# Optimization experiments

Measured on AMD Instinct MI355X. Metric: run time of the kernel, lower is better.

Reference implementation:

```python
import jax, jax.numpy as jnp
import numpy as np
from jax import lax

EPS = 1e-5
DIM = 96      # channels = dim
KS = 96       # kernel_size == H == W
GROUPS = 8
BATCH = 4
FFN_F = 2.66

# relative index table: emb[c, i, j] = rel[c, i - j + KS - 1]
_REL_IDX = (np.arange(KS)[:, None] - np.arange(KS)[None, :] + KS - 1).reshape(-1)


def _bn(x, g, b, ax):
    """BatchNorm (training-mode batch statistics) over all axes except `ax`."""
    axes = tuple(i for i in range(x.ndim) if i != ax)
    m = x.mean(axes, keepdims=True)
    v = x.var(axes, keepdims=True)
    sh = [1] * x.ndim
    sh[ax] = -1
    return (x - m) / jnp.sqrt(v + EPS) * g.reshape(sh) + b.reshape(sh)


def _ln(x, w, b):
    """WithBias LayerNorm over channel dim of NCHW (per-pixel over C)."""
    m = x.mean(1, keepdims=True)
    v = x.var(1, keepdims=True)
    return (x - m) / jnp.sqrt(v + EPS) * w[None, :, None, None] + b[None, :, None, None]


def _axial(x, wqkv, gq, bq, rel, gs, bs, go, bo, width):
    # x: (N, C, H, W)
    xp = x.transpose(0, 2, 1, 3) if width else x.transpose(0, 3, 1, 2)
    N, Wd, C, L = xp.shape
    gp = C // GROUPS  # group_planes
    xb = xp.reshape(N * Wd, C, L)
    qkv = _bn(jnp.einsum('oc,bcl->bol', wqkv, xb), gq, bq, 1)
    qkv = qkv.reshape(N * Wd, GROUPS, 2 * gp, L)
    q, k, v = qkv[:, :, :gp // 2], qkv[:, :, gp // 2:gp], qkv[:, :, gp:]
    emb = rel[:, _REL_IDX].reshape(2 * gp, L, L)
    qe, ke, ve = emb[:gp // 2], emb[gp // 2:gp], emb[gp:]
    qk = jnp.einsum('bgci,bgcj->bgij', q, k)
    qr = jnp.einsum('bgci,cij->bgij', q, qe)
    kr = jnp.einsum('bgci,cij->bgij', k, ke).transpose(0, 1, 3, 2)
    sim = _bn(jnp.concatenate([qk, qr, kr], 1), gs, bs, 1)
    sim = sim.reshape(N * Wd, 3, GROUPS, L, L).sum(1)
    sim = jax.nn.softmax(sim, axis=3)
    sv = jnp.einsum('bgij,bgcj->bgci', sim, v)
    sve = jnp.einsum('bgij,cij->bgci', sim, ve)
    out = _bn(jnp.concatenate([sv, sve], -1).reshape(N * Wd, 2 * C, L), go, bo, 1)
    out = out.reshape(N, Wd, C, 2, L).sum(3)
    return out.transpose(0, 2, 1, 3) if width else out.transpose(0, 2, 3, 1)


def _ffn(x, win, wdw, wout):
    h = jnp.einsum('oc,bchw->bohw', win, x)
    h = lax.conv_general_dilated(h, wdw, (1, 1), 'SAME',
                                 dimension_numbers=('NCHW', 'OIHW', 'NCHW'),
                                 feature_group_count=h.shape[1])
    x1, x2 = jnp.split(h, 2, axis=1)
    return jnp.einsum('oc,bchw->bohw', wout, jax.nn.gelu(x1, approximate=False) * x2)


def setup_inputs() -> dict:
    key = jax.random.key(0)
    ks = jax.random.split(key, 8)
    dim, gp = DIM, DIM // GROUPS
    hid = int(dim * FFN_F)
    f = jax.random.normal
    d = {'x': f(ks[0], (BATCH, dim, KS, KS), jnp.float32)}
    d['ln1_w'] = jnp.ones(dim); d['ln1_b'] = jnp.zeros(dim)
    for p, i in (('h_', 1), ('w_', 2)):
        k1, k2 = jax.random.split(ks[i])
        d[p + 'wqkv'] = f(k1, (2 * dim, dim), jnp.float32) * float(np.sqrt(1.0 / dim))
        d[p + 'gqkv'] = jnp.ones(2 * dim); d[p + 'bqkv'] = jnp.zeros(2 * dim)
        d[p + 'rel'] = f(k2, (2 * gp, 2 * KS - 1), jnp.float32) * float(np.sqrt(1.0 / gp))
        d[p + 'gsim'] = jnp.ones(3 * GROUPS); d[p + 'bsim'] = jnp.zeros(3 * GROUPS)
        d[p + 'gout'] = jnp.ones(2 * dim); d[p + 'bout'] = jnp.zeros(2 * dim)
    d['ln2_w'] = jnp.ones(dim); d['ln2_b'] = jnp.zeros(dim)
    d['ffn_win'] = f(ks[3], (2 * hid, dim), jnp.float32) * float(np.sqrt(1.0 / dim))
    d['ffn_wdw'] = f(ks[4], (2 * hid, 1, 3, 3), jnp.float32) * 0.1
    d['ffn_wout'] = f(ks[5], (dim, hid), jnp.float32) * float(np.sqrt(1.0 / hid))
    return d


def reference(x, ln1_w, ln1_b,
              h_wqkv, h_gqkv, h_bqkv, h_rel, h_gsim, h_bsim, h_gout, h_bout,
              w_wqkv, w_gqkv, w_bqkv, w_rel, w_gsim, w_bsim, w_gout, w_bout,
              ln2_w, ln2_b, ffn_win, ffn_wdw, ffn_wout):
    y = _ln(x, ln1_w, ln1_b)
    y = _axial(y, h_wqkv, h_gqkv, h_bqkv, h_rel, h_gsim, h_bsim, h_gout, h_bout, False)
    y = _axial(y, w_wqkv, w_gqkv, w_bqkv, w_rel, w_gsim, w_bsim, w_gout, w_bout, True)
    x = x + y
    x = x + _ffn(_ln(x, ln2_w, ln2_b), ffn_win, ffn_wdw, ffn_wout)
    return x
```

## Files before the change

### kernel.cpp

```cpp
#include <hip/hip_runtime.h>
#include <hip/hip_bf16.h>
#include <math.h>

using bf16 = __hip_bfloat16;

#define NB 4
#define C_ 96
#define NPIX 36864
#define IMG 9216
#define CH_ST 9216
#define N_ST 884736
#define HID 255
#define EPSF 1e-5f
#define TOT 3538944

__global__ __launch_bounds__(256) void ln_kernel(const float* __restrict__ X,
                                                 float* __restrict__ Y,
                                                 const float* __restrict__ w,
                                                 const float* __restrict__ b) {
  int pix = blockIdx.x * 256 + threadIdx.x;
  if (pix >= NPIX) return;
  int n = pix / IMG, p = pix % IMG;
  const float* xp = X + (long)n * N_ST + p;
  float s = 0.f, sq = 0.f;
  for (int c = 0; c < C_; c++) { float v = xp[c * CH_ST]; s += v; sq += v * v; }
  float m = s * (1.f / C_);
  float var = fmaxf(sq * (1.f / C_) - m * m, 0.f);
  float r = rsqrtf(var + EPSF);
  float* yp = Y + (long)n * N_ST + p;
  for (int c = 0; c < C_; c++)
    yp[c * CH_ST] = (xp[c * CH_ST] - m) * r * w[c] + b[c];
}

__global__ void trans_kernel(const float* __restrict__ Y0, float* __restrict__ Y0C) {
  __shared__ float T[32][33];
  int nc = blockIdx.z; int n = nc / C_, c = nc % C_;
  int h0 = blockIdx.x * 32, w0 = blockIdx.y * 32;
  int tx = threadIdx.x, ty = threadIdx.y;
  const float* src = Y0 + (long)n * N_ST + (long)c * CH_ST;
  for (int r = 0; r < 4; r++)
    T[ty + 8 * r][tx] = src[(h0 + ty + 8 * r) * 96 + w0 + tx];
  __syncthreads();
  float* dst = Y0C + (long)c * NPIX + (long)n * IMG;
  for (int r = 0; r < 4; r++)
    dst[(w0 + ty + 8 * r) * 96 + h0 + tx] = T[tx][ty + 8 * r];
}

template<int TM, int TN, int EPI>
__global__ __launch_bounds__(256) void gemm_kernel(
    const float* __restrict__ A, const float* __restrict__ B,
    float* __restrict__ Cout, int M, int K, int NperZ,
    long bCstride, long bZstride, int batch,
    const float* __restrict__ X1, float* __restrict__ OutF) {
  constexpr int NT = TN / 16;
  constexpr int RT = TM / 16;
  __shared__ float As[32][TM];
  __shared__ float Bs[32][TN + 4];
  const int tx = threadIdx.x, ty = threadIdx.y;
  const int tid = ty * 16 + tx;
  const int m0 = blockIdx.y * TM;
  const int q0 = blockIdx.x * TN;
  const int z  = blockIdx.z;
  const float* Bz = B + (long)z * bZstride;
  float acc[RT][NT];
  #pragma unroll
  for (int a = 0; a < RT; a++)
    #pragma unroll
    for (int b = 0; b < NT; b++) acc[a][b] = 0.f;

  for (int kk = 0; kk < K; kk += 32) {
    #pragma unroll
    for (int it = 0; it < (32 * TM) / 256; it++) {
      int i = tid + it * 256;
      int c = i / TM, r = i % TM;
      int mm = m0 + r, kc = kk + c;
      As[c][r] = (mm < M && kc < K) ? A[(long)mm * K + kc] : 0.f;
    }
    #pragma unroll
    for (int it = 0; it < (32 * TN) / 256; it++) {
      int i = tid + it * 256;
      int c = i / TN, q = i % TN;
      int kc = kk + c;
      Bs[c][q] = (kc < K) ? Bz[(long)kc * bCstride + q0 + q] : 0.f;
    }
    __syncthreads();
    for (int kc = 0; kc < 32; kc++) {
      float av[RT];
      if constexpr (RT % 4 == 0) {
        #pragma unroll
        for (int u = 0; u < RT / 4; u++) {
          float4 a4 = *(const float4*)&As[kc][ty * RT + 4 * u];
          av[4 * u] = a4.x; av[4 * u + 1] = a4.y; av[4 * u + 2] = a4.z; av[4 * u + 3] = a4.w;
        }
      } else {
        #pragma unroll
        for (int u = 0; u < RT / 2; u++) {
          float2 a2 = *(const float2*)&As[kc][ty * RT + 2 * u];
          av[2 * u] = a2.x; av[2 * u + 1] = a2.y;
        }
      }
      float bv[NT];
      #pragma unroll
      for (int v4 = 0; v4 < NT / 4; v4++) {
        float4 b4 = *(const float4*)&Bs[kc][v4 * 64 + tx * 4];
        bv[v4 * 4] = b4.x; bv[v4 * 4 + 1] = b4.y; bv[v4 * 4 + 2] = b4.z; bv[v4 * 4 + 3] = b4.w;
      }
      #pragma unroll
      for (int a = 0; a < RT; a++)
        #pragma unroll
        for (int b = 0; b < NT; b++)
          acc[a][b] = fmaf(av[a], bv[b], acc[a][b]);
    }
    __syncthreads();
  }
  const long oStride = (long)NperZ * gridDim.z;
  if (EPI == 0) {
    #pragma unroll
    for (int a = 0; a < RT; a++) {
      int mm = m0 + ty * RT + a;
      if (mm < M) {
        float* dst = Cout + (long)mm * oStride + (long)z * NperZ + q0;
        #pragma unroll
        for (int v4 = 0; v4 < NT / 4; v4++)
          *(float4*)(dst + v4 * 64 + tx * 4) =
              make_float4(acc[a][v4 * 4], acc[a][v4 * 4 + 1],
                          acc[a][v4 * 4 + 2], acc[a][v4 * 4 + 3]);
      }
    }
  } else {
    #pragma unroll
    for (int a = 0; a < RT; a++) {
      int mm = m0 + ty * RT + a;
      if (mm < M) {
        #pragma unroll
        for (int v4 = 0; v4 < NT / 4; v4++) {
          int Q = q0 + v4 * 64 + tx * 4;
          int n = batch + z + Q / IMG, p = Q % IMG;
          long base = (long)n * N_ST + (long)mm * CH_ST + p;
          #pragma unroll
          for (int b = 0; b < 4; b++)
            OutF[base + b] = acc[a][v4 * 4 + b] + X1[base + b];
        }
      }
    }
  }
}

__global__ __launch_bounds__(1024) void rowstat_kernel(const float* __restrict__ D,
                                                       const float* __restrict__ g,
                                                       const float* __restrict__ b,
                                                       float2* __restrict__ aff) {
  int o = blockIdx.x;
  const float4* p = (const float4*)(D + (long)o * NPIX);
  float s = 0.f, sq = 0.f;
  for (int i = threadIdx.x; i < NPIX / 4; i += 1024) {
    float4 v = p[i];
    s  += v.x + v.y + v.z + v.w;
    sq += v.x * v.x + v.y * v.y + v.z * v.z + v.w * v.w;
  }
  for (int off = 32; off; off >>= 1) { s += __shfl_down(s, off); sq += __shfl_down(sq, off); }
  __shared__ float ss[16], ssq[16];
  int wv = threadIdx.x >> 6, lane = threadIdx.x & 63;
  if (lane == 0) { ss[wv] = s; ssq[wv] = sq; }
  __syncthreads();
  if (threadIdx.x == 0) {
    float S = 0.f, SQ = 0.f;
    #pragma unroll
    for (int i = 0; i < 16; i++) { S += ss[i]; SQ += ssq[i]; }
    float m = S / (float)NPIX;
    float var = fmaxf(SQ / (float)NPIX - m * m, 0.f);
    float sc = g[o] * rsqrtf(var + EPSF);
    aff[o] = make_float2(sc, b[o] - m * sc);
  }
}

__global__ void relstat_kernel(const float* __restrict__ relp, float* __restrict__ tbl) {
  int i = threadIdx.x;
  if (i >= 96) return;
  int side = blockIdx.x / 27, row = blockIdx.x % 27;
  const float* base = relp + side * 6 * 191;
  float* T = tbl + side * 27 * 96;
  if (row < 6) {
    float s = 0.f;
    for (int d = 0; d < 96; d++) s += base[row * 191 + i + d];
    T[row * 96 + i] = s;
  } else {
    int p = row - 6, c = 0;
    while (p >= 6 - c) { p -= 6 - c; c++; }
    int c2 = c + p;
    float s = 0.f;
    for (int d = 0; d < 96; d++) s += base[c * 191 + i + d] * base[c2 * 191 + i + d];
    T[576 + (row - 6) * 96 + i] = s;
  }
}

__global__ __launch_bounds__(256) void simstat2_kernel(const float* __restrict__ QKV,
                                                       const float2* __restrict__ aff,
                                                       const float* __restrict__ tbl,
                                                       float* __restrict__ stats) {
  int g = blockIdx.x & 7, chunk = blockIdx.x >> 3;
  int bbg = threadIdx.x >> 5, lane = threadIdx.x & 31;
  int bb = chunk * 8 + bbg;
  const float* Aq = tbl;
  const float* Wq = tbl + 6 * 96;
  const float* Ak = tbl + 27 * 96;
  const float* Wk = tbl + 27 * 96 + 6 * 96;
  float Sq[6] = {}, Sk[6] = {}, Gq[21] = {}, Gk[21] = {};
  float lq = 0.f, lsq = 0.f, lk = 0.f, lsk = 0.f;
  #pragma unroll
  for (int ii = 0; ii < 3; ii++) {
    int i = lane + 32 * ii;
    float qv[6], kv[6];
    #pragma unroll
    for (int c = 0; c < 6; c++) {
      int oq = g * 24 + c, ok = g * 24 + 6 + c;
      float2 a = aff[oq], b2 = aff[ok];
      qv[c] = QKV[(long)oq * NPIX + bb * 96 + i] * a.x + a.y;
      kv[c] = QKV[(long)ok * NPIX + bb * 96 + i] * b2.x + b2.y;
      Sq[c] += qv[c]; Sk[c] += kv[c];
      lq = fmaf(qv[c], Aq[c * 96 + i], lq);
      lk = fmaf(kv[c], Ak[c * 96 + i], lk);
    }
    int p = 0;
    #pragma unroll
    for (int c = 0; c < 6; c++)
      #pragma unroll
      for (int c2 = c; c2 < 6; c2++, p++) {
        float f = (c == c2) ? 1.f : 2.f;
        float pq = qv[c] * qv[c2], pk = kv[c] * kv[c2];
        Gq[p] += pq; Gk[p] += pk;
        lsq = fmaf(pq * f, Wq[p * 96 + i], lsq);
        lsk = fmaf(pk * f, Wk[p * 96 + i], lsk);
      }
  }
  #pragma unroll
  for (int off = 16; off; off >>= 1) {
    #pragma unroll
    for (int c = 0; c < 6; c++) { Sq[c] += __shfl_down(Sq[c], off, 32); Sk[c] += __shfl_down(Sk[c], off, 32); }
    #pragma unroll
    for (int p = 0; p < 21; p++) { Gq[p] += __shfl_down(Gq[p], off, 32); Gk[p] += __shfl_down(Gk[p], off, 32); }
    lq += __shfl_down(lq, off, 32);  lsq += __shfl_down(lsq, off, 32);
    lk += __shfl_down(lk, off, 32);  lsk += __shfl_down(lsk, off, 32);
  }
  __shared__ float red[6];
  if (threadIdx.x < 6) red[threadIdx.x] = 0.f;
  __syncthreads();
  if (lane == 0) {
    float sqk = 0.f, sqk2 = 0.f;
    #pragma unroll
    for (int c = 0; c < 6; c++) sqk += Sq[c] * Sk[c];
    int p = 0;
    #pragma unroll
    for (int c = 0; c < 6; c++)
      #pragma unroll
      for (int c2 = c; c2 < 6; c2++, p++)
        sqk2 += ((c == c2) ? 1.f : 2.f) * Gq[p] * Gk[p];
    atomicAdd(&red[0], sqk); atomicAdd(&red[3], sqk2);
    atomicAdd(&red[1], lq);  atomicAdd(&red[4], lsq);
    atomicAdd(&red[2], lk);  atomicAdd(&red[5], lsk);
  }
  __syncthreads();
  if (threadIdx.x < 3) {
    atomicAdd(&stats[(threadIdx.x * 8 + g) * 2 + 0], red[threadIdx.x]);
    atomicAdd(&stats[(threadIdx.x * 8 + g) * 2 + 1], red[threadIdx.x + 3]);
  }
}

__global__ void simfin_kernel(const float* __restrict__ stats,
                              const float* __restrict__ gsim,
                              float* __restrict__ scale) {
  int t = threadIdx.x;
  if (t < 24) {
    float cnt = 384.f * 9216.f;
    float m = stats[t * 2] / cnt;
    float var = fmaxf(stats[t * 2 + 1] / cnt - m * m, 0.f);
    scale[t] = gsim[t] * rsqrtf(var + EPSF);
  }
}

__global__ __launch_bounds__(256) void attn_kernel(const float* __restrict__ QKV,
                                                   const float2* __restrict__ aff,
                                                   const float* __restrict__ relp,
                                                   const float* __restrict__ sscale,
                                                   float* __restrict__ OutPre) {
  int blk = blockIdx.x;
  int bb = blk >> 3, g = blk & 7;
  __shared__ float qF[6][96];
  __shared__ float kF[6][96];
  __shared__ float vF[12][96];
  __shared__ float rl[24 * 191];
  __shared__ float P[32][100];
  int tid = threadIdx.x;
  float s0 = sscale[g], s1 = sscale[8 + g], s2 = sscale[16 + g];
  for (int i = tid; i < 288; i += 256) {
    int half = i / 144, r = i % 144;
    int c = r / 24, qd = r % 24;
    int o = g * 24 + half * 6 + c;
    float2 a = aff[o];
    float4 v = *(const float4*)(QKV + (long)o * NPIX + bb * 96 + qd * 4);
    float4 w = make_float4(v.x * a.x + a.y, v.y * a.x + a.y,
                           v.z * a.x + a.y, v.w * a.x + a.y);
    if (half == 0) *(float4*)&qF[c][qd * 4] = w;
    else           *(float4*)&kF[c][qd * 4] = w;
  }
  for (int i = tid; i < 288; i += 256) {
    int c = i / 24, qd = i % 24;
    int o = g * 24 + 12 + c;
    float2 a = aff[o];
    float4 v = *(const float4*)(QKV + (long)o * NPIX + bb * 96 + qd * 4);
    *(float4*)&vF[c][qd * 4] = make_float4(v.x * a.x + a.y, v.y * a.x + a.y,
                                           v.z * a.x + a.y, v.w * a.x + a.y);
  }
  for (int i = tid; i < 1146; i += 256) {
    int e = i * 4;
    float4 v = *(const float4*)(relp + e);
    float4 w;
    w.x = v.x * ((e + 0) < 1146 ? s1 : (e + 0) < 2292 ? s2 : 1.f);
    w.y = v.y * ((e + 1) < 1146 ? s1 : (e + 1) < 2292 ? s2 : 1.f);
    w.z = v.z * ((e + 2) < 1146 ? s1 : (e + 2) < 2292 ? s2 : 1.f);
    w.w = v.w * ((e + 3) < 1146 ? s1 : (e + 3) < 2292 ? s2 : 1.f);
    *(float4*)&rl[e] = w;
  }
  __syncthreads();
  int hw = tid >> 5, l32 = tid & 31;
  for (int iq = 0; iq < 3; iq++) {
    int i0 = iq * 32;
    {
      int til = hw * 4;
      int ti = i0 + til;
      int tj = l32 * 3;
      int d0 = ti - tj + 93;
      int e0 = tj - ti + 92;
      float ap[4][3] = {};
      #pragma unroll
      for (int c = 0; c < 6; c++) {
        float4 q4 = *(const float4*)&qF[c][ti];
        float qv[4] = {q4.x, q4.y, q4.z, q4.w};
        float kv[3], kv0[3], rq[6], rk[6];
        #pragma unroll
        for (int j = 0; j < 3; j++) { kv[j] = kF[c][tj + j]; kv0[j] = s0 * kv[j]; }
        #pragma unroll
        for (int u = 0; u < 6; u++) { rq[u] = rl[c * 191 + d0 + u]; rk[u] = rl[(6 + c) * 191 + e0 + u]; }
        #pragma unroll
        for (int ii = 0; ii < 4; ii++)
          #pragma unroll
          for (int jj = 0; jj < 3; jj++) {
            ap[ii][jj] = fmaf(qv[ii], kv0[jj], ap[ii][jj]);
            ap[ii][jj] = fmaf(qv[ii], rq[ii - jj + 2], ap[ii][jj]);
            ap[ii][jj] = fmaf(kv[jj], rk[jj - ii + 3], ap[ii][jj]);
          }
      }
      #pragma unroll
      for (int ii = 0; ii < 4; ii++)
        #pragma unroll
        for (int jj = 0; jj < 3; jj++)
          P[til + ii][l32 * 3 + jj] = ap[ii][jj];
    }
    __syncthreads();
    for (int r = hw; r < 32; r += 8) {
      float v0 = P[r][l32], v1 = P[r][l32 + 32], v2 = P[r][l32 + 64];
      float mx = fmaxf(v0, fmaxf(v1, v2));
      #pragma unroll
      for (int off = 16; off; off >>= 1) mx = fmaxf(mx, __shfl_xor(mx, off, 32));
      float e0 = __expf(v0 - mx), e1 = __expf(v1 - mx), e2 = __expf(v2 - mx);
      P[r][l32] = e0; P[r][l32 + 32] = e1; P[r][l32 + 64] = e2;
      float s = e0 + e1 + e2;
      #pragma unroll
      for (int off = 16; off; off >>= 1) s += __shfl_xor(s, off, 32);
      if (l32 == 0) P[r][96] = 1.f / s;
    }
    __syncthreads();
    {
      int orr0 = hw * 3;
      float acc3[3] = {};
      for (int jq = 0; jq < 24; jq++) {
        int j0 = jq * 4;
        float4 pv = *(const float4*)&P[l32][j0];
        #pragma unroll
        for (int u = 0; u < 3; u++) {
          int orr = orr0 + u, cc = orr >> 1;
          if ((orr & 1) == 0) {
            float4 vv = *(const float4*)&vF[cc][j0];
            acc3[u] += pv.x * vv.x + pv.y * vv.y + pv.z * vv.z + pv.w * vv.w;
          } else {
            const float* rv = &rl[(12 + cc) * 191];
            int bse = (i0 + l32) - j0 + 92;
            float f0 = rv[bse], f1 = rv[bse + 1], f2 = rv[bse + 2], f3 = rv[bse + 3];
            acc3[u] += pv.w * f0 + pv.z * f1 + pv.y * f2 + pv.x * f3;
          }
        }
      }
      float ri = P[l32][96];
      #pragma unroll
      for (int u = 0; u < 3; u++)
        OutPre[(long)(g * 24 + orr0 + u) * NPIX + bb * 96 + i0 + l32] = acc3[u] * ri;
    }
    __syncthreads();
  }
}

__global__ void apply1_kernel(const float* __restrict__ OutPre,
                              const float2* __restrict__ aff,
                              float* __restrict__ Y1) {
  __shared__ float T[32][33];
  int z = blockIdx.z; int n = z / C_, cf = z % C_;
  int h0 = blockIdx.x * 32, w0 = blockIdx.y * 32;
  int tx = threadIdx.x, ty = threadIdx.y;
  float2 a0 = aff[2 * cf], a1 = aff[2 * cf + 1];
  const float* r0 = OutPre + (long)(2 * cf) * NPIX + (long)n * IMG;
  const float* r1 = OutPre + (long)(2 * cf + 1) * NPIX + (long)n * IMG;
  for (int r = 0; r < 4; r++) {
    int w = w0 + ty + 8 * r;
    int idx = w * 96 + h0 + tx;
    T[ty + 8 * r][tx] = (r0[idx] * a0.x + a0.y) + (r1[idx] * a1.x + a1.y);
  }
  __syncthreads();
  float* dst = Y1 + (long)n * N_ST + (long)cf * CH_ST;
  for (int r = 0; r < 4; r++)
    dst[(h0 + ty + 8 * r) * 96 + w0 + tx] = T[tx][ty + 8 * r];
}

__global__ __launch_bounds__(256) void apply2_kernel(const float* __restrict__ OutPre,
                                                     const float2* __restrict__ aff,
                                                     const float* __restrict__ X,
                                                     float* __restrict__ X1out) {
  int idx = blockIdx.x * 256 + threadIdx.x;
  if (idx >= TOT) return;
  int n = idx / N_ST;
  int rem = idx % N_ST;
  int cf = rem / CH_ST;
  int p = rem % CH_ST;
  long off = (long)n * IMG + p;
  float2 a0 = aff[2 * cf], a1 = aff[2 * cf + 1];
  float v = OutPre[(long)(2 * cf) * NPIX + off] * a0.x + a0.y
          + OutPre[(long)(2 * cf + 1) * NPIX + off] * a1.x + a1.y
          + X[idx];
  X1out[idx] = v;
}

__global__ __launch_bounds__(256) void dwglu_kernel(const float* __restrict__ H,
                                                    const float* __restrict__ Wdw,
                                                    float* __restrict__ Gout) {
  int idx = blockIdx.x * 256 + threadIdx.x;
  if (idx >= HID * IMG) return;
  int c = idx / IMG;
  int p = idx % IMG, y = p / 96, x = p % 96;
  const float* h1 = H + (long)c * IMG;
  const float* h2 = H + (long)(c + HID) * IMG;
  const float* w1 = Wdw + c * 9;
  const float* w2 = Wdw + (c + HID) * 9;
  float acc1 = 0.f, acc2 = 0.f;
  #pragma unroll
  for (int dy = -1; dy <= 1; dy++) {
    int yy = y + dy; if (yy < 0 || yy >= 96) continue;
    #pragma unroll
    for (int dx = -1; dx <= 1; dx++) {
      int xx = x + dx; if (xx < 0 || xx >= 96) continue;
      int wi = (dy + 1) * 3 + dx + 1;
      acc1 = fmaf(h1[yy * 96 + xx], w1[wi], acc1);
      acc2 = fmaf(h2[yy * 96 + xx], w2[wi], acc2);
    }
  }
  float ge = 0.5f * acc1 * (1.f + erff(acc1 * 0.70710678118654752f));
  Gout[idx] = ge * acc2;
}

extern "C" void kernel_launch(void* const* d_in, const int* in_sizes, int n_in,
                              void* d_out, int out_size, void* d_ws, size_t ws_size,
                              hipStream_t stream) {
  const float* x       = (const float*)d_in[0];
  const float* ln1w    = (const float*)d_in[1];
  const float* ln1b    = (const float*)d_in[2];
  const float* h_wqkv  = (const float*)d_in[3];
  const float* h_gqkv  = (const float*)d_in[4];
  const float* h_bqkv  = (const float*)d_in[5];
  const float* h_rel   = (const float*)d_in[6];
  const float* h_gsim  = (const float*)d_in[7];
  const float* h_gout  = (const float*)d_in[9];
  const float* h_bout  = (const float*)d_in[10];
  const float* w_wqkv  = (const float*)d_in[11];
  const float* w_gqkv  = (const float*)d_in[12];
  const float* w_bqkv  = (const float*)d_in[13];
  const float* w_rel   = (const float*)d_in[14];
  const float* w_gsim  = (const float*)d_in[15];
  const float* w_gout  = (const float*)d_in[17];
  const float* w_bout  = (const float*)d_in[18];
  const float* ln2w    = (const float*)d_in[19];
  const float* ln2b    = (const float*)d_in[20];
  const float* ffn_win = (const float*)d_in[21];
  const float* ffn_wdw = (const float*)d_in[22];
  const float* ffn_wout= (const float*)d_in[23];
  float* out = (float*)d_out;

  float* ws = (float*)d_ws;
  float* P = ws;
  float* Q = ws + 3538944;
  float* R = ws + 7077888;
  float* S = ws + 14155776;
  float* Gall = R;
  float* Hbuf = ws + 16478208;
  float* stats = ws + 21233664;
  const size_t need_bytes = (21233664ull + 8192ull) * 4ull;
  if (ws_size < need_bytes) return;

  float2* qkv_aff = (float2*)stats;
  float2* out_aff = (float2*)(stats + 384);
  float*  sim_st  = stats + 768;
  float*  sim_sc  = stats + 864;
  float*  tbl     = stats + 1024;

  hipMemsetAsync(sim_st, 0, 96 * sizeof(float), stream);

  dim3 b256(256), b1616(16, 16), b328(32, 8);

  ln_kernel<<<144, b256, 0, stream>>>(x, P, ln1w, ln1b);
  trans_kernel<<<dim3(3, 3, 384), b328, 0, stream>>>(P, Q);

  gemm_kernel<96, 128, 0><<<dim3(288, 2, 1), b1616, 0, stream>>>(h_wqkv, Q, R,
      192, 96, 36864, 36864L, 0L, 0, nullptr, nullptr);
  rowstat_kernel<<<192, 1024, 0, stream>>>(R, h_gqkv, h_bqkv, qkv_aff);
  relstat_kernel<<<54, 96, 0, stream>>>(h_rel, tbl);
  simstat2_kernel<<<384, b256, 0, stream>>>(R, qkv_aff, tbl, sim_st);
  simfin_kernel<<<1, 32, 0, stream>>>(sim_st, h_gsim, sim_sc);
  attn_kernel<<<3072, b256, 0, stream>>>(R, qkv_aff, h_rel, sim_sc, S);
  rowstat_kernel<<<192, 1024, 0, stream>>>(S, h_gout, h_bout, out_aff);
  apply1_kernel<<<dim3(3, 3, 384), b328, 0, stream>>>(S, out_aff, P);

  gemm_kernel<96, 128, 0><<<dim3(72, 2, 4), b1616, 0, stream>>>(w_wqkv, P, R,
      192, 96, 9216, 9216L, 884736L, 0, nullptr, nullptr);
  rowstat_kernel<<<192, 1024, 0, stream>>>(R, w_gqkv, w_bqkv, qkv_aff);
  relstat_kernel<<<54, 96, 0, stream>>>(w_rel, tbl);
  simstat2_kernel<<<384, b256, 0, stream>>>(R, qkv_aff, tbl, sim_st + 48);
  simfin_kernel<<<1, 32, 0, stream>>>(sim_st + 48, w_gsim, sim_sc + 24);
  attn_kernel<<<3072, b256, 0, stream>>>(R, qkv_aff, w_rel, sim_sc + 24, S);
  rowstat_kernel<<<192, 1024, 0, stream>>>(S, w_gout, w_bout, out_aff);
  apply2_kernel<<<13824, b256, 0, stream>>>(S, out_aff, x, P);

  ln_kernel<<<144, b256, 0, stream>>>(P, Q, ln2w, ln2b);
  for (int n = 0; n < NB; n++) {
    gemm_kernel<128, 64, 0><<<dim3(144, 4, 1), b1616, 0, stream>>>(ffn_win, Q + (long)n * N_ST, Hbuf,
        510, 96, 9216, 9216L, 0L, 0, nullptr, nullptr);
    dwglu_kernel<<<9180, b256, 0, stream>>>(Hbuf, ffn_wdw, Gall + (long)n * 2350080);
  }
  gemm_kernel<96, 64, 1><<<dim3(144, 1, 4), b1616, 0, stream>>>(ffn_wout, Gall, nullptr,
      96, 255, 9216, 9216L, 2350080L, 0, P, out);
}
```

Baseline: 950.1 us.

## Fuse BatchNorm row statistics into GEMM and attention epilogues, drop rowstat passes

Removes the four rowstat kernels that each re-read a 192x36864 buffer. The GEMM epilogue and the attention output stage now accumulate per-channel sum and sum of squares with warp shuffles and atomics, and consumers derive the affine BN coefficients from those sums on the fly. Buffer zeroing is folded into relstat and apply1. It also parallelises LayerNorm across channel quarters with shared-memory reduction, keeps K values in registers in attention, and vectorises the softmax. In exchange it adds atomic contention and makes float summation order nondeterministic.

```diff
diff --git a/kernel.cpp b/kernel.cpp
--- a/kernel.cpp
+++ b/kernel.cpp
@@ -13,23 +13,37 @@
 #define HID 255
 #define EPSF 1e-5f
 #define TOT 3538944
+#define RNPIX (1.f / 36864.f)
 
 __global__ __launch_bounds__(256) void ln_kernel(const float* __restrict__ X,
                                                  float* __restrict__ Y,
                                                  const float* __restrict__ w,
                                                  const float* __restrict__ b) {
-  int pix = blockIdx.x * 256 + threadIdx.x;
-  if (pix >= NPIX) return;
+  __shared__ float red[2][4][64];
+  __shared__ float wb[192];
+  int tid = threadIdx.x;
+  if (tid < 192) wb[tid] = (tid < 96) ? w[tid] : b[tid - 96];
+  int cq = tid >> 6, px = tid & 63;
+  int pix = blockIdx.x * 64 + px;
   int n = pix / IMG, p = pix % IMG;
-  const float* xp = X + (long)n * N_ST + p;
+  const float* xp = X + (long)n * N_ST + (long)(cq * 24) * CH_ST + p;
+  float xr[24];
   float s = 0.f, sq = 0.f;
-  for (int c = 0; c < C_; c++) { float v = xp[c * CH_ST]; s += v; sq += v * v; }
-  float m = s * (1.f / C_);
-  float var = fmaxf(sq * (1.f / C_) - m * m, 0.f);
-  float r = rsqrtf(var + EPSF);
-  float* yp = Y + (long)n * N_ST + p;
-  for (int c = 0; c < C_; c++)
-    yp[c * CH_ST] = (xp[c * CH_ST] - m) * r * w[c] + b[c];
+  #pragma unroll
+  for (int k = 0; k < 24; k++) {
+    float v = xp[(long)k * CH_ST];
+    xr[k] = v; s += v; sq += v * v;
+  }
+  red[0][cq][px] = s; red[1][cq][px] = sq;
+  __syncthreads();
+  float S  = red[0][0][px] + red[0][1][px] + red[0][2][px] + red[0][3][px];
+  float SQ = red[1][0][px] + red[1][1][px] + red[1][2][px] + red[1][3][px];
+  float m = S * (1.f / C_);
+  float r = rsqrtf(fmaxf(SQ * (1.f / C_) - m * m, 0.f) + EPSF);
+  float* yp = Y + (long)n * N_ST + (long)(cq * 24) * CH_ST + p;
+  #pragma unroll
+  for (int k = 0; k < 24; k++)
+    yp[(long)k * CH_ST] = (xr[k] - m) * r * wb[cq * 24 + k] + wb[96 + cq * 24 + k];
 }
 
 __global__ void trans_kernel(const float* __restrict__ Y0, float* __restrict__ Y0C) {
@@ -46,12 +60,13 @@
     dst[(w0 + ty + 8 * r) * 96 + h0 + tx] = T[tx][ty + 8 * r];
 }
 
-template<int TM, int TN, int EPI>
+template<int TM, int TN, int EPI, int STATS>
 __global__ __launch_bounds__(256) void gemm_kernel(
     const float* __restrict__ A, const float* __restrict__ B,
     float* __restrict__ Cout, int M, int K, int NperZ,
     long bCstride, long bZstride, int batch,
-    const float* __restrict__ X1, float* __restrict__ OutF) {
+    const float* __restrict__ X1, float* __restrict__ OutF,
+    float* __restrict__ rsum) {
   constexpr int NT = TN / 16;
   constexpr int RT = TM / 16;
   __shared__ float As[32][TM];
@@ -144,38 +159,30 @@
       }
     }
   }
-}
-
-__global__ __launch_bounds__(1024) void rowstat_kernel(const float* __restrict__ D,
-                                                       const float* __restrict__ g,
-                                                       const float* __restrict__ b,
-                                                       float2* __restrict__ aff) {
-  int o = blockIdx.x;
-  const float4* p = (const float4*)(D + (long)o * NPIX);
-  float s = 0.f, sq = 0.f;
-  for (int i = threadIdx.x; i < NPIX / 4; i += 1024) {
-    float4 v = p[i];
-    s  += v.x + v.y + v.z + v.w;
-    sq += v.x * v.x + v.y * v.y + v.z * v.z + v.w * v.w;
-  }
-  for (int off = 32; off; off >>= 1) { s += __shfl_down(s, off); sq += __shfl_down(sq, off); }
-  __shared__ float ss[16], ssq[16];
-  int wv = threadIdx.x >> 6, lane = threadIdx.x & 63;
-  if (lane == 0) { ss[wv] = s; ssq[wv] = sq; }
-  __syncthreads();
-  if (threadIdx.x == 0) {
-    float S = 0.f, SQ = 0.f;
-    #pragma unroll
-    for (int i = 0; i < 16; i++) { S += ss[i]; SQ += ssq[i]; }
-    float m = S / (float)NPIX;
-    float var = fmaxf(SQ / (float)NPIX - m * m, 0.f);
-    float sc = g[o] * rsqrtf(var + EPSF);
-    aff[o] = make_float2(sc, b[o] - m * sc);
-  }
-}
-
-__global__ void relstat_kernel(const float* __restrict__ relp, float* __restrict__ tbl) {
+  if (STATS) {
+    #pragma unroll
+    for (int a = 0; a < RT; a++) {
+      int mm = m0 + ty * RT + a;
+      float s = 0.f, sq = 0.f;
+      #pragma unroll
+      for (int b = 0; b < NT; b++) { float v = acc[a][b]; s += v; sq += v * v; }
+      #pragma unroll
+      for (int off = 8; off; off >>= 1) {
+        s += __shfl_down(s, off, 16); sq += __shfl_down(sq, off, 16);
+      }
+      if (tx == 0 && mm < M) {
+        atomicAdd(&rsum[mm], s);
+        atomicAdd(&rsum[192 + mm], sq);
+      }
+    }
+  }
+}
+
+__global__ void relstat_kernel(const float* __restrict__ relp, float* __restrict__ tbl,
+                               float* __restrict__ osum) {
   int i = threadIdx.x;
+  if (blockIdx.x == 0)
+    for (int t = i; t < 384; t += 96) osum[t] = 0.f;
   if (i >= 96) return;
   int side = blockIdx.x / 27, row = blockIdx.x % 27;
   const float* base = relp + side * 6 * 191;
@@ -195,7 +202,9 @@
 }
 
 __global__ __launch_bounds__(256) void simstat2_kernel(const float* __restrict__ QKV,
-                                                       const float2* __restrict__ aff,
+                                                       const float* __restrict__ qsum,
+                                                       const float* __restrict__ gq,
+                                                       const float* __restrict__ bq,
                                                        const float* __restrict__ tbl,
                                                        float* __restrict__ stats) {
   int g = blockIdx.x & 7, chunk = blockIdx.x >> 3;
@@ -205,6 +214,17 @@
   const float* Wq = tbl + 6 * 96;
   const float* Ak = tbl + 27 * 96;
   const float* Wk = tbl + 27 * 96 + 6 * 96;
+  float qa[6], qb[6], ka[6], kb[6];
+  #pragma unroll
+  for (int c = 0; c < 6; c++) {
+    int oq = g * 24 + c, ok = g * 24 + 6 + c;
+    float m1 = qsum[oq] * RNPIX;
+    float v1 = fmaxf(qsum[192 + oq] * RNPIX - m1 * m1, 0.f);
+    qa[c] = gq[oq] * rsqrtf(v1 + EPSF); qb[c] = bq[oq] - m1 * qa[c];
+    float m2 = qsum[ok] * RNPIX;
+    float v2 = fmaxf(qsum[192 + ok] * RNPIX - m2 * m2, 0.f);
+    ka[c] = gq[ok] * rsqrtf(v2 + EPSF); kb[c] = bq[ok] - m2 * ka[c];
+  }
   float Sq[6] = {}, Sk[6] = {}, Gq[21] = {}, Gk[21] = {};
   float lq = 0.f, lsq = 0.f, lk = 0.f, lsk = 0.f;
   #pragma unroll
@@ -214,9 +234,8 @@
     #pragma unroll
     for (int c = 0; c < 6; c++) {
       int oq = g * 24 + c, ok = g * 24 + 6 + c;
-      float2 a = aff[oq], b2 = aff[ok];
-      qv[c] = QKV[(long)oq * NPIX + bb * 96 + i] * a.x + a.y;
-      kv[c] = QKV[(long)ok * NPIX + bb * 96 + i] * b2.x + b2.y;
+      qv[c] = QKV[(long)oq * NPIX + bb * 96 + i] * qa[c] + qb[c];
+      kv[c] = QKV[(long)ok * NPIX + bb * 96 + i] * ka[c] + kb[c];
       Sq[c] += qv[c]; Sk[c] += kv[c];
       lq = fmaf(qv[c], Aq[c * 96 + i], lq);
       lk = fmaf(kv[c], Ak[c * 96 + i], lk);
@@ -279,9 +298,12 @@
 }
 
 __global__ __launch_bounds__(256) void attn_kernel(const float* __restrict__ QKV,
-                                                   const float2* __restrict__ aff,
+                                                   const float* __restrict__ qsum,
+                                                   const float* __restrict__ gq,
+                                                   const float* __restrict__ bq,
                                                    const float* __restrict__ relp,
                                                    const float* __restrict__ sscale,
+                                                   float* __restrict__ osum,
                                                    float* __restrict__ OutPre) {
   int blk = blockIdx.x;
   int bb = blk >> 3, g = blk & 7;
@@ -290,13 +312,22 @@
   __shared__ float vF[12][96];
   __shared__ float rl[24 * 191];
   __shared__ float P[32][100];
+  __shared__ float2 aff_s[24];
   int tid = threadIdx.x;
   float s0 = sscale[g], s1 = sscale[8 + g], s2 = sscale[16 + g];
+  if (tid < 24) {
+    int o = g * 24 + tid;
+    float m = qsum[o] * RNPIX;
+    float var = fmaxf(qsum[192 + o] * RNPIX - m * m, 0.f);
+    float sc = gq[o] * rsqrtf(var + EPSF);
+    aff_s[tid] = make_float2(sc, bq[o] - m * sc);
+  }
+  __syncthreads();
   for (int i = tid; i < 288; i += 256) {
     int half = i / 144, r = i % 144;
     int c = r / 24, qd = r % 24;
+    float2 a = aff_s[half * 6 + c];
     int o = g * 24 + half * 6 + c;
-    float2 a = aff[o];
     float4 v = *(const float4*)(QKV + (long)o * NPIX + bb * 96 + qd * 4);
     float4 w = make_float4(v.x * a.x + a.y, v.y * a.x + a.y,
                            v.z * a.x + a.y, v.w * a.x + a.y);
@@ -305,8 +336,8 @@
   }
   for (int i = tid; i < 288; i += 256) {
     int c = i / 24, qd = i % 24;
+    float2 a = aff_s[12 + c];
     int o = g * 24 + 12 + c;
-    float2 a = aff[o];
     float4 v = *(const float4*)(QKV + (long)o * NPIX + bb * 96 + qd * 4);
     *(float4*)&vF[c][qd * 4] = make_float4(v.x * a.x + a.y, v.y * a.x + a.y,
                                            v.z * a.x + a.y, v.w * a.x + a.y);
@@ -323,6 +354,11 @@
   }
   __syncthreads();
   int hw = tid >> 5, l32 = tid & 31;
+  float kreg[6][3];
+  #pragma unroll
+  for (int c = 0; c < 6; c++)
+    #pragma unroll
+    for (int j = 0; j < 3; j++) kreg[c][j] = kF[c][l32 * 3 + j];
   for (int iq = 0; iq < 3; iq++) {
     int i0 = iq * 32;
     {
@@ -336,9 +372,9 @@
       for (int c = 0; c < 6; c++) {
         float4 q4 = *(const float4*)&qF[c][ti];
         float qv[4] = {q4.x, q4.y, q4.z, q4.w};
-        float kv[3], kv0[3], rq[6], rk[6];
-        #pragma unroll
-        for (int j = 0; j < 3; j++) { kv[j] = kF[c][tj + j]; kv0[j] = s0 * kv[j]; }
+        float kv0[3], rq[6], rk[6];
+        #pragma unroll
+        for (int j = 0; j < 3; j++) kv0[j] = s0 * kreg[c][j];
         #pragma unroll
         for (int u = 0; u < 6; u++) { rq[u] = rl[c * 191 + d0 + u]; rk[u] = rl[(6 + c) * 191 + e0 + u]; }
         #pragma unroll
@@ -347,7 +383,7 @@
           for (int jj = 0; jj < 3; jj++) {
             ap[ii][jj] = fmaf(qv[ii], kv0[jj], ap[ii][jj]);
             ap[ii][jj] = fmaf(qv[ii], rq[ii - jj + 2], ap[ii][jj]);
-            ap[ii][jj] = fmaf(kv[jj], rk[jj - ii + 3], ap[ii][jj]);
+            ap[ii][jj] = fmaf(kreg[c][jj], rk[jj - ii + 3], ap[ii][jj]);
           }
       }
       #pragma unroll
@@ -357,17 +393,29 @@
           P[til + ii][l32 * 3 + jj] = ap[ii][jj];
     }
     __syncthreads();
-    for (int r = hw; r < 32; r += 8) {
-      float v0 = P[r][l32], v1 = P[r][l32 + 32], v2 = P[r][l32 + 64];
-      float mx = fmaxf(v0, fmaxf(v1, v2));
-      #pragma unroll
-      for (int off = 16; off; off >>= 1) mx = fmaxf(mx, __shfl_xor(mx, off, 32));
-      float e0 = __expf(v0 - mx), e1 = __expf(v1 - mx), e2 = __expf(v2 - mx);
-      P[r][l32] = e0; P[r][l32 + 32] = e1; P[r][l32 + 64] = e2;
-      float s = e0 + e1 + e2;
-      #pragma unroll
-      for (int off = 16; off; off >>= 1) s += __shfl_xor(s, off, 32);
-      if (l32 == 0) P[r][96] = 1.f / s;
+    {
+      int wv = tid >> 6, rloc = (tid >> 3) & 7, l8 = tid & 7;
+      int r = wv * 8 + rloc;
+      float* Pr = &P[r][l8 * 12];
+      float4 v0 = *(const float4*)(Pr);
+      float4 v1 = *(const float4*)(Pr + 4);
+      float4 v2 = *(const float4*)(Pr + 8);
+      float mx = fmaxf(fmaxf(fmaxf(v0.x, v0.y), fmaxf(v0.z, v0.w)),
+                 fmaxf(fmaxf(fmaxf(v1.x, v1.y), fmaxf(v1.z, v1.w)),
+                       fmaxf(fmaxf(v2.x, v2.y), fmaxf(v2.z, v2.w))));
+      #pragma unroll
+      for (int off = 4; off; off >>= 1) mx = fmaxf(mx, __shfl_xor(mx, off, 8));
+      v0 = make_float4(__expf(v0.x - mx), __expf(v0.y - mx), __expf(v0.z - mx), __expf(v0.w - mx));
+      v1 = make_float4(__expf(v1.x - mx), __expf(v1.y - mx), __expf(v1.z - mx), __expf(v1.w - mx));
+      v2 = make_float4(__expf(v2.x - mx), __expf(v2.y - mx), __expf(v2.z - mx), __expf(v2.w - mx));
+      float s = v0.x + v0.y + v0.z + v0.w + v1.x + v1.y + v1.z + v1.w
+              + v2.x + v2.y + v2.z + v2.w;
+      #pragma unroll
+      for (int off = 4; off; off >>= 1) s += __shfl_xor(s, off, 8);
+      *(float4*)(Pr)     = v0;
+      *(float4*)(Pr + 4) = v1;
+      *(float4*)(Pr + 8) = v2;
+      if (l8 == 0) P[r][96] = 1.f / s;
     }
     __syncthreads();
     {
@@ -392,27 +440,50 @@
       }
       float ri = P[l32][96];
       #pragma unroll
-      for (int u = 0; u < 3; u++)
-        OutPre[(long)(g * 24 + orr0 + u) * NPIX + bb * 96 + i0 + l32] = acc3[u] * ri;
+      for (int u = 0; u < 3; u++) {
+        float ov = acc3[u] * ri;
+        OutPre[(long)(g * 24 + orr0 + u) * NPIX + bb * 96 + i0 + l32] = ov;
+        float sv = ov, sqv = ov * ov;
+        #pragma unroll
+        for (int off = 16; off; off >>= 1) {
+          sv += __shfl_down(sv, off, 32); sqv += __shfl_down(sqv, off, 32);
+        }
+        if (l32 == 0) {
+          atomicAdd(&osum[g * 24 + orr0 + u], sv);
+          atomicAdd(&osum[192 + g * 24 + orr0 + u], sqv);
+        }
+      }
     }
     __syncthreads();
   }
 }
 
 __global__ void apply1_kernel(const float* __restrict__ OutPre,
-                              const float2* __restrict__ aff,
+                              const float* __restrict__ osum,
+                              const float* __restrict__ gout,
+                              const float* __restrict__ bout,
+                              float* __restrict__ qsum,
                               float* __restrict__ Y1) {
   __shared__ float T[32][33];
+  int tx = threadIdx.x, ty = threadIdx.y;
+  if (blockIdx.x == 0 && blockIdx.y == 0 && blockIdx.z == 0) {
+    for (int t = ty * 32 + tx; t < 384; t += 256) qsum[t] = 0.f;
+  }
   int z = blockIdx.z; int n = z / C_, cf = z % C_;
   int h0 = blockIdx.x * 32, w0 = blockIdx.y * 32;
-  int tx = threadIdx.x, ty = threadIdx.y;
-  float2 a0 = aff[2 * cf], a1 = aff[2 * cf + 1];
-  const float* r0 = OutPre + (long)(2 * cf) * NPIX + (long)n * IMG;
-  const float* r1 = OutPre + (long)(2 * cf + 1) * NPIX + (long)n * IMG;
+  int o0 = 2 * cf, o1 = 2 * cf + 1;
+  float m0 = osum[o0] * RNPIX;
+  float a0x = gout[o0] * rsqrtf(fmaxf(osum[192 + o0] * RNPIX - m0 * m0, 0.f) + EPSF);
+  float a0y = bout[o0] - m0 * a0x;
+  float m1 = osum[o1] * RNPIX;
+  float a1x = gout[o1] * rsqrtf(fmaxf(osum[192 + o1] * RNPIX - m1 * m1, 0.f) + EPSF);
+  float a1y = bout[o1] - m1 * a1x;
+  const float* r0 = OutPre + (long)o0 * NPIX + (long)n * IMG;
+  const float* r1 = OutPre + (long)o1 * NPIX + (long)n * IMG;
   for (int r = 0; r < 4; r++) {
     int w = w0 + ty + 8 * r;
     int idx = w * 96 + h0 + tx;
-    T[ty + 8 * r][tx] = (r0[idx] * a0.x + a0.y) + (r1[idx] * a1.x + a1.y);
+    T[ty + 8 * r][tx] = (r0[idx] * a0x + a0y) + (r1[idx] * a1x + a1y);
   }
   __syncthreads();
   float* dst = Y1 + (long)n * N_ST + (long)cf * CH_ST;
@@ -421,7 +492,9 @@
 }
 
 __global__ __launch_bounds__(256) void apply2_kernel(const float* __restrict__ OutPre,
-                                                     const float2* __restrict__ aff,
+                                                     const float* __restrict__ osum,
+                                                     const float* __restrict__ gout,
+                                                     const float* __restrict__ bout,
                                                      const float* __restrict__ X,
                                                      float* __restrict__ X1out) {
   int idx = blockIdx.x * 256 + threadIdx.x;
@@ -431,9 +504,15 @@
   int cf = rem / CH_ST;
   int p = rem % CH_ST;
   long off = (long)n * IMG + p;
-  float2 a0 = aff[2 * cf], a1 = aff[2 * cf + 1];
-  float v = OutPre[(long)(2 * cf) * NPIX + off] * a0.x + a0.y
-          + OutPre[(long)(2 * cf + 1) * NPIX + off] * a1.x + a1.y
+  int o0 = 2 * cf, o1 = 2 * cf + 1;
+  float m0 = osum[o0] * RNPIX;
+  float a0x = gout[o0] * rsqrtf(fmaxf(osum[192 + o0] * RNPIX - m0 * m0, 0.f) + EPSF);
+  float a0y = bout[o0] - m0 * a0x;
+  float m1 = osum[o1] * RNPIX;
+  float a1x = gout[o1] * rsqrtf(fmaxf(osum[192 + o1] * RNPIX - m1 * m1, 0.f) + EPSF);
+  float a1y = bout[o1] - m1 * a1x;
+  float v = OutPre[(long)o0 * NPIX + off] * a0x + a0y
+          + OutPre[(long)o1 * NPIX + off] * a1x + a1y
           + X[idx];
   X1out[idx] = v;
 }
@@ -503,45 +582,41 @@
   const size_t need_bytes = (21233664ull + 8192ull) * 4ull;
   if (ws_size < need_bytes) return;
 
-  float2* qkv_aff = (float2*)stats;
-  float2* out_aff = (float2*)(stats + 384);
-  float*  sim_st  = stats + 768;
-  float*  sim_sc  = stats + 864;
-  float*  tbl     = stats + 1024;
-
-  hipMemsetAsync(sim_st, 0, 96 * sizeof(float), stream);
+  float* qkv_sum = stats;
+  float* out_sum = stats + 384;
+  float* sim_st  = stats + 768;
+  float* sim_sc  = stats + 864;
+  float* tbl     = stats + 1024;
+
+  hipMemsetAsync(stats, 0, 8192 * sizeof(float), stream);
 
   dim3 b256(256), b1616(16, 16), b328(32, 8);
 
-  ln_kernel<<<144, b256, 0, stream>>>(x, P, ln1w, ln1b);
+  ln_kernel<<<576, b256, 0, stream>>>(x, P, ln1w, ln1b);
   trans_kernel<<<dim3(3, 3, 384), b328, 0, stream>>>(P, Q);
 
-  gemm_kernel<96, 128, 0><<<dim3(288, 2, 1), b1616, 0, stream>>>(h_wqkv, Q, R,
-      192, 96, 36864, 36864L, 0L, 0, nullptr, nullptr);
-  rowstat_kernel<<<192, 1024, 0, stream>>>(R, h_gqkv, h_bqkv, qkv_aff);
-  relstat_kernel<<<54, 96, 0, stream>>>(h_rel, tbl);
-  simstat2_kernel<<<384, b256, 0, stream>>>(R, qkv_aff, tbl, sim_st);
+  gemm_kernel<96, 128, 0, 1><<<dim3(288, 2, 1), b1616, 0, stream>>>(h_wqkv, Q, R,
+      192, 96, 36864, 36864L, 0L, 0, nullptr, nullptr, qkv_sum);
+  relstat_kernel<<<54, 96, 0, stream>>>(h_rel, tbl, out_sum);
+  simstat2_kernel<<<384, b256, 0, stream>>>(R, qkv_sum, h_gqkv, h_bqkv, tbl, sim_st);
   simfin_kernel<<<1, 32, 0, stream>>>(sim_st, h_gsim, sim_sc);
-  attn_kernel<<<3072, b256, 0, stream>>>(R, qkv_aff, h_rel, sim_sc, S);
-  rowstat_kernel<<<192, 1024, 0, stream>>>(S, h_gout, h_bout, out_aff);
-  apply1_kernel<<<dim3(3, 3, 384), b328, 0, stream>>>(S, out_aff, P);
-
-  gemm_kernel<96, 128, 0><<<dim3(72, 2, 4), b1616, 0, stream>>>(w_wqkv, P, R,
-      192, 96, 9216, 9216L, 884736L, 0, nullptr, nullptr);
-  rowstat_kernel<<<192, 1024, 0, stream>>>(R, w_gqkv, w_bqkv, qkv_aff);
-  relstat_kernel<<<54, 96, 0, stream>>>(w_rel, tbl);
-  simstat2_kernel<<<384, b256, 0, stream>>>(R, qkv_aff, tbl, sim_st + 48);
+  attn_kernel<<<3072, b256, 0, stream>>>(R, qkv_sum, h_gqkv, h_bqkv, h_rel, sim_sc, out_sum, S);
+  apply1_kernel<<<dim3(3, 3, 384), b328, 0, stream>>>(S, out_sum, h_gout, h_bout, qkv_sum, P);
+
+  gemm_kernel<96, 128, 0, 1><<<dim3(72, 2, 4), b1616, 0, stream>>>(w_wqkv, P, R,
+      192, 96, 9216, 9216L, 884736L, 0, nullptr, nullptr, qkv_sum);
+  relstat_kernel<<<54, 96, 0, stream>>>(w_rel, tbl, out_sum);
+  simstat2_kernel<<<384, b256, 0, stream>>>(R, qkv_sum, w_gqkv, w_bqkv, tbl, sim_st + 48);
   simfin_kernel<<<1, 32, 0, stream>>>(sim_st + 48, w_gsim, sim_sc + 24);
-  attn_kernel<<<3072, b256, 0, stream>>>(R, qkv_aff, w_rel, sim_sc + 24, S);
-  rowstat_kernel<<<192, 1024, 0, stream>>>(S, w_gout, w_bout, out_aff);
-  apply2_kernel<<<13824, b256, 0, stream>>>(S, out_aff, x, P);
-
-  ln_kernel<<<144, b256, 0, stream>>>(P, Q, ln2w, ln2b);
+  attn_kernel<<<3072, b256, 0, stream>>>(R, qkv_sum, w_gqkv, w_bqkv, w_rel, sim_sc + 24, out_sum, S);
+  apply2_kernel<<<13824, b256, 0, stream>>>(S, out_sum, w_gout, w_bout, x, P);
+
+  ln_kernel<<<576, b256, 0, stream>>>(P, Q, ln2w, ln2b);
   for (int n = 0; n < NB; n++) {
-    gemm_kernel<128, 64, 0><<<dim3(144, 4, 1), b1616, 0, stream>>>(ffn_win, Q + (long)n * N_ST, Hbuf,
-        510, 96, 9216, 9216L, 0L, 0, nullptr, nullptr);
+    gemm_kernel<128, 64, 0, 0><<<dim3(144, 4, 1), b1616, 0, stream>>>(ffn_win, Q + (long)n * N_ST, Hbuf,
+        510, 96, 9216, 9216L, 0L, 0, nullptr, nullptr, nullptr);
     dwglu_kernel<<<9180, b256, 0, stream>>>(Hbuf, ffn_wdw, Gall + (long)n * 2350080);
   }
-  gemm_kernel<96, 64, 1><<<dim3(144, 1, 4), b1616, 0, stream>>>(ffn_wout, Gall, nullptr,
-      96, 255, 9216, 9216L, 2350080L, 0, P, out);
-}
+  gemm_kernel<96, 64, 1, 0><<<dim3(144, 1, 4), b1616, 0, stream>>>(ffn_wout, Gall, nullptr,
+      96, 255, 9216, 9216L, 2350080L, 0, P, out, nullptr);
+}
```

Result: slower. 1.351 ms (+42.2%).
